# Performance work log

Hardware: AMD Instinct MI355X
Metric: run time of the kernel (lower is better)

The kernel has to match this reference:

```python
import jax, jax.numpy as jnp
import numpy as np

N_ENT = 50000; N_REL = 200; D = 128; HEADS = 2; ATT_D = 64
E_FULL = 300000; E_BATCH = 80000; NEG_SLOPE = 0.2


def _leaky(x, ns):
    return jnp.where(x >= 0, x, ns * x)


def _gat_conv(x, src, dst, ea, W, We, att_s, att_d, att_e, bias, neg_slope=0.2):
    """PyG GATConv with edge features, add_self_loops=True (fill_value='mean')."""
    N = x.shape[0]
    H, C = att_s.shape
    E = src.shape[0]
    # self-loop edge_attr = mean of incoming edge_attrs per node (PyG fill_value='mean')
    deg = jax.ops.segment_sum(jnp.ones((E,), x.dtype), dst, num_segments=N)
    ea_loop = jax.ops.segment_sum(ea, dst, num_segments=N) / jnp.maximum(deg, 1.0)[:, None]
    loops = jnp.arange(N, dtype=src.dtype)
    src2 = jnp.concatenate([src, loops])
    dst2 = jnp.concatenate([dst, loops])
    ea2 = jnp.concatenate([ea, ea_loop], axis=0)            # [E+N, edge_dim]
    xt = (x @ W).reshape(N, H, C)                            # [N,H,C]
    et = (ea2 @ We).reshape(-1, H, C)                        # [E+N,H,C]
    a_src = jnp.einsum('nhc,hc->nh', xt, att_s)
    a_dst = jnp.einsum('nhc,hc->nh', xt, att_d)
    a_edge = jnp.einsum('ehc,hc->eh', et, att_e)
    alpha = a_src[src2] + a_dst[dst2] + a_edge               # [E+N,H]
    alpha = _leaky(alpha, neg_slope)
    # segment softmax over edges sharing the same target node
    amax = jax.ops.segment_max(alpha, dst2, num_segments=N)
    ex = jnp.exp(alpha - amax[dst2])
    den = jax.ops.segment_sum(ex, dst2, num_segments=N)
    alpha = ex / (den[dst2] + 1e-16)
    out = jax.ops.segment_sum(xt[src2] * alpha[:, :, None], dst2, num_segments=N)
    return out.reshape(N, H * C) + bias


def setup_inputs() -> dict:
    key = jax.random.key(0)
    ks = list(jax.random.split(key, 24))
    p = lambda k, s: jax.random.normal(k, s, dtype=jnp.float32) * 0.05
    s = jax.random.randint(ks[0], (E_FULL,), 0, N_ENT, dtype=jnp.int32)
    r = jax.random.randint(ks[1], (E_FULL,), 0, N_REL, dtype=jnp.int32)
    t = jax.random.randint(ks[2], (E_FULL,), 0, N_ENT, dtype=jnp.int32)
    edge_data = jnp.stack([s, r, t], axis=0)
    edge_index = jax.random.randint(ks[3], (2, E_BATCH), 0, N_ENT, dtype=jnp.int32)
    rel_ids = jax.random.randint(ks[4], (E_BATCH,), 0, N_REL, dtype=jnp.int32)
    edge_attr = jax.nn.one_hot(rel_ids, N_REL, dtype=jnp.float32)
    H1 = HEADS * ATT_D
    H2 = HEADS * D
    return {
        'edge_index': edge_index, 'edge_attr': edge_attr, 'edge_data': edge_data,
        'ent_emb': p(ks[5], (N_ENT, D)), 'rel_emb': p(ks[6], (N_REL, D)),
        'W1': p(ks[7], (D, H1)), 'We1': p(ks[8], (D, H1)),
        'att_s1': p(ks[9], (HEADS, ATT_D)), 'att_d1': p(ks[10], (HEADS, ATT_D)),
        'att_e1': p(ks[11], (HEADS, ATT_D)), 'b1': jnp.zeros((H1,), jnp.float32),
        'W2': p(ks[12], (H1, H2)), 'We2': p(ks[13], (D, H2)),
        'att_s2': p(ks[14], (HEADS, D)), 'att_d2': p(ks[15], (HEADS, D)),
        'att_e2': p(ks[16], (HEADS, D)), 'b2': jnp.zeros((H2,), jnp.float32),
        'W_skip': p(ks[17], (D, D)), 'W_r': p(ks[18], (D, N_REL)),
    }


def reference(edge_index, edge_attr, edge_data, ent_emb, rel_emb, W1, We1, att_s1, att_d1, att_e1, b1, W2, We2, att_s2, att_d2, att_e2, b2, W_skip, W_r):
    src, rel, dst = edge_data[0], edge_data[1], edge_data[2]
    ea = rel_emb[rel]                                        # [E_FULL, D]
    x = _gat_conv(ent_emb, src, dst, ea, W1, We1, att_s1, att_d1, att_e1, b1)
    x = _leaky(x, NEG_SLOPE)                                 # inter-layer act
    x = _gat_conv(x, src, dst, ea, W2, We2, att_s2, att_d2, att_e2, b2)
    # mean over head chunks: [N, H*D] -> [N, D]
    x = x.reshape(N_ENT, HEADS, D).mean(axis=1)
    x = x + ent_emb @ W_skip.T                               # skip connection
    x = x / jnp.maximum(jnp.linalg.norm(x, axis=1, keepdims=True), 1e-12)
    edge_emb = jnp.stack([x[edge_index[0]], x[edge_index[1]]], axis=0)  # [2,EB,D]
    edge_attr_out = edge_attr @ W_r.T                        # [EB, D]
    return edge_emb, edge_attr_out
```

## Files before the change

kernel.cpp:

```cpp
#include <hip/hip_runtime.h>

#define NE 50000
#define NR 200
#define EF 300000
#define EB 80000
#define NEG 0.2f
#define NINF (-1e30f)

typedef unsigned short u16;
typedef unsigned int u32;
typedef u16 u16x8 __attribute__((ext_vector_type(8)));
typedef __bf16 bf16x8 __attribute__((ext_vector_type(8)));
typedef float f32x4 __attribute__((ext_vector_type(4)));

__device__ __forceinline__ float lrelu(float x){ return x >= 0.f ? x : NEG*x; }
__device__ __forceinline__ u16 f2bf(float f){
  unsigned u = __float_as_uint(f);
  u = (u + 0x7FFFu + ((u >> 16) & 1u)) >> 16;
  return (u16)u;
}
__device__ __forceinline__ float bf2f(u16 u){ return __uint_as_float(((unsigned)u) << 16); }
__device__ __forceinline__ float bflo(u32 p){ return __uint_as_float(p << 16); }
__device__ __forceinline__ float bfhi(u32 p){ return __uint_as_float(p & 0xFFFF0000u); }

__global__ void k_count(const int* __restrict__ edge_data, int* __restrict__ cnt){
  int e = blockIdx.x*blockDim.x + threadIdx.x;
  if(e < EF) atomicAdd(&cnt[edge_data[2*EF + e]], 1);
}

__global__ void k_scan(const int* __restrict__ cnt, int* __restrict__ row_start){
  __shared__ int wsum[16];
  __shared__ int s_run;
  int tid = threadIdx.x;
  int lane = tid & 63, wv = tid >> 6;
  if(tid==0) s_run = 0;
  __syncthreads();
  const int CH = 4096;
  const int nch = (NE + CH - 1)/CH;
  for(int c=0;c<nch;c++){
    int base = c*CH + tid*4;
    int v0 = base   < NE ? cnt[base]   : 0;
    int v1 = base+1 < NE ? cnt[base+1] : 0;
    int v2 = base+2 < NE ? cnt[base+2] : 0;
    int v3 = base+3 < NE ? cnt[base+3] : 0;
    int tsum = v0+v1+v2+v3;
    int x = tsum;
    #pragma unroll
    for(int o=1;o<64;o<<=1){
      int y = __shfl_up(x, o);
      if(lane >= o) x += y;
    }
    if(lane==63) wsum[wv] = x;
    __syncthreads();
    if(wv==0 && lane<16){
      int w = wsum[lane];
      #pragma unroll
      for(int o=1;o<16;o<<=1){
        int y = __shfl_up(w, o);
        if(lane>=o) w += y;
      }
      wsum[lane] = w;
    }
    __syncthreads();
    int woff = (wv>0) ? wsum[wv-1] : 0;
    int excl = s_run + woff + x - tsum;
    if(base   < NE) row_start[base]   = excl;
    if(base+1 < NE) row_start[base+1] = excl + v0;
    if(base+2 < NE) row_start[base+2] = excl + v0+v1;
    if(base+3 < NE) row_start[base+3] = excl + v0+v1+v2;
    __syncthreads();
    if(tid==1023) s_run += wsum[15];
    __syncthreads();
  }
  if(tid==0) row_start[NE] = s_run;
}

__global__ void k_fill(const int* __restrict__ edge_data, const int* __restrict__ row_start,
                       int* __restrict__ cnt, int* __restrict__ src_s, int* __restrict__ rel_s){
  int e = blockIdx.x*blockDim.x + threadIdx.x;
  if(e < EF){
    int s = edge_data[e], r = edge_data[EF+e], d = edge_data[2*EF+e];
    int pos = row_start[d] + atomicAdd(&cnt[d], 1);
    src_s[pos] = s; rel_s[pos] = r;
  }
}

__global__ void k_vecE(const float* __restrict__ We1, const float* __restrict__ ae1,
                       const float* __restrict__ We2, const float* __restrict__ ae2,
                       float* __restrict__ vecE1, float* __restrict__ vecE2){
  int t = threadIdx.x;
  int d = t>>1, h = t&1;
  float s1 = 0.f;
  for(int c=0;c<64;c++)  s1 += We1[d*128 + h*64  + c]*ae1[h*64  + c];
  vecE1[d*2+h] = s1;
  float s2 = 0.f;
  for(int c=0;c<128;c++) s2 += We2[d*256 + h*128 + c]*ae2[h*128 + c];
  vecE2[d*2+h] = s2;
}

__global__ void k_aE(const float* __restrict__ rel_emb, const float* __restrict__ vecE1,
                     const float* __restrict__ vecE2, float* __restrict__ aE1, float* __restrict__ aE2){
  int r = blockIdx.x, l = threadIdx.x;
  float re0 = rel_emb[r*128 + l], re1 = rel_emb[r*128 + 64 + l];
  float a10 = re0*vecE1[l*2+0] + re1*vecE1[(64+l)*2+0];
  float a11 = re0*vecE1[l*2+1] + re1*vecE1[(64+l)*2+1];
  float a20 = re0*vecE2[l*2+0] + re1*vecE2[(64+l)*2+0];
  float a21 = re0*vecE2[l*2+1] + re1*vecE2[(64+l)*2+1];
  for(int o=32;o;o>>=1){
    a10 += __shfl_xor(a10,o); a11 += __shfl_xor(a11,o);
    a20 += __shfl_xor(a20,o); a21 += __shfl_xor(a21,o);
  }
  if(l==0){ aE1[r*2]=a10; aE1[r*2+1]=a11; aE2[r*2]=a20; aE2[r*2+1]=a21; }
}

__global__ void k_tr(const float* __restrict__ A, float* __restrict__ At, int R, int C){
  int t = blockIdx.x*blockDim.x + threadIdx.x;
  if(t < R*C){ int r = t / C, c = t % C; At[c*R + r] = A[t]; }
}

__global__ void k_prep(const float* __restrict__ W1, const float* __restrict__ Wsk,
                       const float* __restrict__ W2, u16* __restrict__ WT1s, u16* __restrict__ WT2){
  int r = blockIdx.x, k = threadIdx.x;
  if(r < 128)       WT1s[r*128+k] = f2bf(W1[k*128 + r]);
  else if(r < 256)  WT1s[r*128+k] = f2bf(Wsk[(r-128)*128 + k]);
  else              WT2[(r-256)*128+k] = f2bf(W2[k*256 + (r-256)]);
}

template<bool XBF, bool SPLIT>
__global__ __launch_bounds__(256) void k_mgemm(const void* __restrict__ Xv,
    const u16* __restrict__ WT, u16* __restrict__ Y0, u16* __restrict__ Yb, int Nrows){
  __shared__ u16 As[64*128];
  __shared__ u16 Bs[64*128];
  int n0 = blockIdx.x*64;
  int t  = threadIdx.x;
  #pragma unroll
  for(int i=0;i<4;i++){
    int c = i*256 + t;
    int row = c >> 4, kc = c & 15;
    u16x8 pk;
    if(XBF){
      const u16* Xb = (const u16*)Xv;
      if(n0+row < Nrows) pk = *reinterpret_cast<const u16x8*>(&Xb[(size_t)(n0+row)*128 + kc*8]);
      else               pk = (u16x8)(u16)0;
    } else {
      const float* Xf = (const float*)Xv;
      float4 v0 = make_float4(0,0,0,0), v1 = v0;
      if(n0+row < Nrows){
        const float4* p = reinterpret_cast<const float4*>(&Xf[(size_t)(n0+row)*128 + kc*8]);
        v0 = p[0]; v1 = p[1];
      }
      pk[0]=f2bf(v0.x); pk[1]=f2bf(v0.y); pk[2]=f2bf(v0.z); pk[3]=f2bf(v0.w);
      pk[4]=f2bf(v1.x); pk[5]=f2bf(v1.y); pk[6]=f2bf(v1.z); pk[7]=f2bf(v1.w);
    }
    *reinterpret_cast<u16x8*>(&As[row*128 + ((kc ^ (row&7))<<3)]) = pk;
  }
  int l = t & 63, w = t >> 6;
  int wr = w >> 1, wc = w & 1;
  int lr = l & 15, kg = l >> 4;
  const bf16x8* asp = reinterpret_cast<const bf16x8*>(As);
  const bf16x8* bsp = reinterpret_cast<const bf16x8*>(Bs);
  for(int cbi=0; cbi<4; cbi++){
    int cb = cbi*64;
    #pragma unroll
    for(int i=0;i<4;i++){
      int c = i*256 + t;
      int row = c >> 4, kc = c & 15;
      u16x8 pk = *reinterpret_cast<const u16x8*>(&WT[(size_t)(cb+row)*128 + kc*8]);
      *reinterpret_cast<u16x8*>(&Bs[row*128 + ((kc ^ (row&7))<<3)]) = pk;
    }
    __syncthreads();
    f32x4 acc[2][2] = {};
    #pragma unroll
    for(int kk=0; kk<4; kk++){
      bf16x8 a[2], b[2];
      #pragma unroll
      for(int m=0;m<2;m++){
        int fr = wr*32 + m*16 + lr;
        a[m] = asp[fr*16 + ((kk*4 + kg) ^ (fr&7))];
      }
      #pragma unroll
      for(int n=0;n<2;n++){
        int fc = wc*32 + n*16 + lr;
        b[n] = bsp[fc*16 + ((kk*4 + kg) ^ (fc&7))];
      }
      #pragma unroll
      for(int m=0;m<2;m++)
        #pragma unroll
        for(int n=0;n<2;n++)
          acc[m][n] = __builtin_amdgcn_mfma_f32_16x16x32_bf16(a[m], b[n], acc[m][n], 0, 0, 0);
    }
    #pragma unroll
    for(int m=0;m<2;m++){
      #pragma unroll
      for(int r=0;r<4;r++){
        int grow = n0 + wr*32 + m*16 + kg*4 + r;
        if(grow < Nrows){
          #pragma unroll
          for(int n=0;n<2;n++){
            int gcol = cb + wc*32 + n*16 + lr;
            u16 v = f2bf(acc[m][n][r]);
            if(SPLIT){
              if(cb >= 128) Yb[(size_t)grow*128 + (gcol-128)] = v;
              else          Y0[(size_t)grow*128 + gcol] = v;
            } else {
              Y0[(size_t)grow*256 + gcol] = v;
            }
          }
        }
      }
    }
    __syncthreads();
  }
}

template<int C>
__global__ void k_attn(const u16* __restrict__ xt, const float* __restrict__ att_s,
                       const float* __restrict__ att_d, float* __restrict__ asrc,
                       float* __restrict__ adst){
  int wv = threadIdx.x>>6, l = threadIdx.x&63;
  int n = blockIdx.x*4 + wv;
  if(n >= NE) return;
  const u32* row = reinterpret_cast<const u32*>(xt) + (size_t)n*C;
  if(C==64){
    u32 p = row[l];
    float x0 = bflo(p), x1 = bfhi(p);
    float sl = x0*att_s[2*l] + x1*att_s[2*l+1];
    float dl = x0*att_d[2*l] + x1*att_d[2*l+1];
    #pragma unroll
    for(int o=16;o;o>>=1){ sl += __shfl_xor(sl,o); dl += __shfl_xor(dl,o); }
    if(l==0){  asrc[n*2]   = sl; adst[n*2]   = dl; }
    if(l==32){ asrc[n*2+1] = sl; adst[n*2+1] = dl; }
  } else {
    u32 p0 = row[l], p1 = row[64+l];
    float x00 = bflo(p0), x01 = bfhi(p0), x10 = bflo(p1), x11 = bfhi(p1);
    float s0 = x00*att_s[2*l]     + x01*att_s[2*l+1];
    float s1 = x10*att_s[128+2*l] + x11*att_s[128+2*l+1];
    float d0 = x00*att_d[2*l]     + x01*att_d[2*l+1];
    float d1 = x10*att_d[128+2*l] + x11*att_d[128+2*l+1];
    #pragma unroll
    for(int o=32;o;o>>=1){
      s0+=__shfl_xor(s0,o); s1+=__shfl_xor(s1,o);
      d0+=__shfl_xor(d0,o); d1+=__shfl_xor(d1,o);
    }
    if(l==0){ asrc[n*2]=s0; asrc[n*2+1]=s1; adst[n*2]=d0; adst[n*2+1]=d1; }
  }
}

template<int C, bool LK, bool OUTBF>
__global__ __launch_bounds__(256) void k_agg(const u16* __restrict__ xt,
    const float* __restrict__ asrc, const float* __restrict__ adst,
    const float* __restrict__ aE, const int* __restrict__ row_start,
    const int* __restrict__ src_s, const int* __restrict__ rel_s,
    const float* __restrict__ bias, void* __restrict__ outv){
  constexpr int NP = C/64;
  __shared__ float2 sAE[NR];
  int tid = threadIdx.x;
  for(int i=tid; i<NR; i+=256) sAE[i] = reinterpret_cast<const float2*>(aE)[i];
  __syncthreads();
  int wv = tid>>6, l = tid&63;
  int n = blockIdx.x*4 + wv;
  if(n >= NE) return;
  int b = row_start[n], e = row_start[n+1];
  int deg = e - b;
  float2 ad  = *reinterpret_cast<const float2*>(&adst[n*2]);
  float2 asn = *reinterpret_cast<const float2*>(&asrc[n*2]);
  const u32* xtu = reinterpret_cast<const u32*>(xt);
  float m0=NINF, m1=NINF, den0=0.f, den1=0.f, sE0=0.f, sE1=0.f;
  float acc[NP][2];
  #pragma unroll
  for(int j=0;j<NP;j++){ acc[j][0]=0.f; acc[j][1]=0.f; }
  for(int i=b;i<e;i++){
    int s = src_s[i], r = rel_s[i];
    float2 as = *reinterpret_cast<const float2*>(&asrc[s*2]);
    float2 ae = sAE[r];
    sE0 += ae.x; sE1 += ae.y;
    float l0 = lrelu(as.x + ad.x + ae.x);
    float l1 = lrelu(as.y + ad.y + ae.y);
    float nm0 = fmaxf(m0,l0), nm1 = fmaxf(m1,l1);
    float sc0 = __expf(m0-nm0), sc1 = __expf(m1-nm1);
    float w0  = __expf(l0-nm0), w1  = __expf(l1-nm1);
    den0 = den0*sc0 + w0; den1 = den1*sc1 + w1;
    m0 = nm0; m1 = nm1;
    #pragma unroll
    for(int j=0;j<NP;j++){
      u32 p = xtu[(size_t)s*C + j*64 + l];
      float sc, w;
      if(C==64){ sc = (l<32)?sc0:sc1; w = (l<32)?w0:w1; }
      else     { sc = (j==0)?sc0:sc1; w = (j==0)?w0:w1; }
      acc[j][0] = acc[j][0]*sc + w*bflo(p);
      acc[j][1] = acc[j][1]*sc + w*bfhi(p);
    }
  }
  {
    float invdeg = 1.f/fmaxf((float)deg, 1.f);
    float l0 = lrelu(asn.x + ad.x + sE0*invdeg);
    float l1 = lrelu(asn.y + ad.y + sE1*invdeg);
    float nm0 = fmaxf(m0,l0), nm1 = fmaxf(m1,l1);
    float sc0 = __expf(m0-nm0), sc1 = __expf(m1-nm1);
    float w0  = __expf(l0-nm0), w1  = __expf(l1-nm1);
    den0 = den0*sc0 + w0; den1 = den1*sc1 + w1;
    #pragma unroll
    for(int j=0;j<NP;j++){
      u32 p = xtu[(size_t)n*C + j*64 + l];
      float sc, w;
      if(C==64){ sc = (l<32)?sc0:sc1; w = (l<32)?w0:w1; }
      else     { sc = (j==0)?sc0:sc1; w = (j==0)?w0:w1; }
      acc[j][0] = acc[j][0]*sc + w*bflo(p);
      acc[j][1] = acc[j][1]*sc + w*bfhi(p);
    }
  }
  float i0 = 1.f/(den0 + 1e-16f), i1 = 1.f/(den1 + 1e-16f);
  #pragma unroll
  for(int j=0;j<NP;j++){
    float ih;
    if(C==64) ih = (l<32)?i0:i1; else ih = (j==0)?i0:i1;
    float2 bp = reinterpret_cast<const float2*>(bias)[j*64 + l];
    float v0 = acc[j][0]*ih + bp.x;
    float v1 = acc[j][1]*ih + bp.y;
    if(LK){ v0 = lrelu(v0); v1 = lrelu(v1); }
    if(OUTBF){
      ((u32*)outv)[(size_t)n*C + j*64 + l] = (u32)f2bf(v0) | ((u32)f2bf(v1)<<16);
    } else {
      reinterpret_cast<float2*>(outv)[(size_t)n*(C) + j*64 + l] = make_float2(v0, v1);
    }
  }
}

__global__ void k_combine(const float* __restrict__ out2, const u16* __restrict__ skip,
                          u16* __restrict__ xf){
  int wv = threadIdx.x>>6, l = threadIdx.x&63;
  int n = blockIdx.x*4 + wv;
  if(n >= NE) return;
  const float2* o2 = reinterpret_cast<const float2*>(out2) + (size_t)n*128;
  float2 a0 = o2[l], a1 = o2[64+l];
  u32 sp = reinterpret_cast<const u32*>(skip)[(size_t)n*64 + l];
  float v0 = 0.5f*(a0.x + a1.x) + bflo(sp);
  float v1 = 0.5f*(a0.y + a1.y) + bfhi(sp);
  float ss = v0*v0 + v1*v1;
  for(int o=32;o;o>>=1) ss += __shfl_xor(ss,o);
  float inv = 1.f/fmaxf(sqrtf(ss), 1e-12f);
  reinterpret_cast<u32*>(xf)[(size_t)n*64 + l] = (u32)f2bf(v0*inv) | ((u32)f2bf(v1*inv)<<16);
}

__global__ void k_gather(const int* __restrict__ ei, const u16* __restrict__ xf,
                         float* __restrict__ out){
  int wv = threadIdx.x>>6, l = threadIdx.x&63;
  int e = blockIdx.x*4 + wv;
  if(e >= EB) return;
  int i0 = ei[e], i1 = ei[EB + e];
  u32 p0 = reinterpret_cast<const u32*>(xf)[(size_t)i0*64 + l];
  u32 p1 = reinterpret_cast<const u32*>(xf)[(size_t)i1*64 + l];
  reinterpret_cast<float2*>(out)[(size_t)e*64 + l] = make_float2(bflo(p0), bfhi(p0));
  reinterpret_cast<float2*>(out + (size_t)EB*128)[(size_t)e*64 + l] = make_float2(bflo(p1), bfhi(p1));
}

__global__ void k_attr(const float* __restrict__ ea, const float* __restrict__ Wrt,
                       float* __restrict__ out){
  int wv = threadIdx.x>>6, l = threadIdx.x&63;
  int e = blockIdx.x*4 + wv;
  if(e >= EB) return;
  const float* row = ea + (size_t)e*NR;
  float acc0=0.f, acc1=0.f;
  #pragma unroll
  for(int ch=0; ch<4; ch++){
    int idx = ch*64 + l;
    float v = (idx < NR) ? row[idx] : 0.f;
    unsigned long long mask = __ballot(v != 0.f);
    while(mask){
      int bit = __builtin_ctzll(mask);
      mask &= mask - 1;
      int r = ch*64 + bit;
      float vv = __shfl(v, bit);
      acc0 += vv * Wrt[r*128 + l];
      acc1 += vv * Wrt[r*128 + 64 + l];
    }
  }
  out[(size_t)e*128 + l]      = acc0;
  out[(size_t)e*128 + 64 + l] = acc1;
}

extern "C" void kernel_launch(void* const* d_in, const int* in_sizes, int n_in,
                              void* d_out, int out_size, void* d_ws, size_t ws_size,
                              hipStream_t stream){
  const int*   edge_index = (const int*)  d_in[0];
  const float* edge_attr  = (const float*)d_in[1];
  const int*   edge_data  = (const int*)  d_in[2];
  const float* ent_emb    = (const float*)d_in[3];
  const float* rel_emb    = (const float*)d_in[4];
  const float* W1     = (const float*)d_in[5];
  const float* att_s1 = (const float*)d_in[7];
  const float* att_d1 = (const float*)d_in[8];
  const float* att_e1 = (const float*)d_in[9];
  const float* b1     = (const float*)d_in[10];
  const float* W2     = (const float*)d_in[11];
  const float* We1    = (const float*)d_in[6];
  const float* We2    = (const float*)d_in[12];
  const float* att_s2 = (const float*)d_in[13];
  const float* att_d2 = (const float*)d_in[14];
  const float* att_e2 = (const float*)d_in[15];
  const float* b2     = (const float*)d_in[16];
  const float* W_skip = (const float*)d_in[17];
  const float* W_r    = (const float*)d_in[18];
  float* out = (float*)d_out;

  char* ws = (char*)d_ws;
  size_t off = 0;
  auto alloc = [&](size_t bytes){ void* p = ws + off; off += (bytes + 255) & ~(size_t)255; return p; };
  int*   cnt       = (int*)  alloc((size_t)NE*4);
  int*   row_start = (int*)  alloc((size_t)(NE+1)*4);
  int*   src_s     = (int*)  alloc((size_t)EF*4);
  int*   rel_s     = (int*)  alloc((size_t)EF*4);
  float* vecE1     = (float*)alloc(128*2*4);
  float* vecE2     = (float*)alloc(128*2*4);
  float* aE1       = (float*)alloc(NR*2*4);
  float* aE2       = (float*)alloc(NR*2*4);
  float* asrc1     = (float*)alloc((size_t)NE*2*4);
  float* adst1     = (float*)alloc((size_t)NE*2*4);
  float* asrc2     = (float*)alloc((size_t)NE*2*4);
  float* adst2     = (float*)alloc((size_t)NE*2*4);
  u16*   WT1s      = (u16*)  alloc(256*128*2);
  u16*   WT2       = (u16*)  alloc(256*128*2);
  float* Wrt       = (float*)alloc(NR*128*4);
  u16*   xt1       = (u16*)  alloc((size_t)NE*128*2);
  u16*   skip      = (u16*)  alloc((size_t)NE*128*2);
  u16*   h1        = (u16*)  alloc((size_t)NE*128*2);
  u16*   xf = xt1;
  u16*   xt2  = (u16*)out;
  float* out2 = out + (size_t)NE*128;

  hipMemsetAsync(cnt, 0, (size_t)NE*4, stream);
  k_count<<<(EF+255)/256, 256, 0, stream>>>(edge_data, cnt);
  k_scan<<<1, 1024, 0, stream>>>(cnt, row_start);
  hipMemsetAsync(cnt, 0, (size_t)NE*4, stream);
  k_fill<<<(EF+255)/256, 256, 0, stream>>>(edge_data, row_start, cnt, src_s, rel_s);
  k_vecE<<<1, 256, 0, stream>>>(We1, att_e1, We2, att_e2, vecE1, vecE2);
  k_aE<<<NR, 64, 0, stream>>>(rel_emb, vecE1, vecE2, aE1, aE2);
  k_prep<<<512, 128, 0, stream>>>(W1, W_skip, W2, WT1s, WT2);
  k_tr<<<(128*NR+255)/256, 256, 0, stream>>>(W_r, Wrt, 128, NR);

  int gg = (NE+63)/64;
  k_mgemm<false, true><<<gg, 256, 0, stream>>>(ent_emb, WT1s, xt1, skip, NE);
  k_attn<64><<<(NE+3)/4, 256, 0, stream>>>(xt1, att_s1, att_d1, asrc1, adst1);
  k_agg<64, true, true><<<(NE+3)/4, 256, 0, stream>>>(xt1, asrc1, adst1, aE1, row_start, src_s, rel_s, b1, h1);

  k_mgemm<true, false><<<gg, 256, 0, stream>>>(h1, WT2, xt2, nullptr, NE);
  k_attn<128><<<(NE+3)/4, 256, 0, stream>>>(xt2, att_s2, att_d2, asrc2, adst2);
  k_agg<128, false, false><<<(NE+3)/4, 256, 0, stream>>>(xt2, asrc2, adst2, aE2, row_start, src_s, rel_s, b2, out2);

  k_combine<<<(NE+3)/4, 256, 0, stream>>>(out2, skip, xf);

  k_gather<<<(EB+3)/4, 256, 0, stream>>>(edge_index, xf, out);
  k_attr<<<(EB+3)/4, 256, 0, stream>>>(edge_attr, Wrt, out + (size_t)2*EB*128);
}
```

Baseline: 492.0 us.

## Aggregate raw features before projection and fold attention vectors into weights

The GAT layers are reordered so neighbor aggregation runs on the 128-wide input features, one output per head, and the per-head projection is applied afterwards as a K=256 MFMA GEMM. Attention logits come from precomputed W·att vectors, so the separate attention-score kernels and the transformed-feature gathers go away. The head-mean, bias, skip connection and L2 normalisation are fused into the last GEMM's epilogue. The online-softmax max tracking is dropped and raw exp is used, which risks overflow if logits grow large.

```diff
diff --git a/kernel.cpp b/kernel.cpp
--- a/kernel.cpp
+++ b/kernel.cpp
@@ -5,7 +5,6 @@
 #define EF 300000
 #define EB 80000
 #define NEG 0.2f
-#define NINF (-1e30f)
 
 typedef unsigned short u16;
 typedef unsigned int u32;
@@ -22,6 +21,7 @@
 __device__ __forceinline__ float bf2f(u16 u){ return __uint_as_float(((unsigned)u) << 16); }
 __device__ __forceinline__ float bflo(u32 p){ return __uint_as_float(p << 16); }
 __device__ __forceinline__ float bfhi(u32 p){ return __uint_as_float(p & 0xFFFF0000u); }
+__device__ __forceinline__ u32 pack2(float a, float b){ return (u32)f2bf(a) | ((u32)f2bf(b)<<16); }
 
 __global__ void k_count(const int* __restrict__ edge_data, int* __restrict__ cnt){
   int e = blockIdx.x*blockDim.x + threadIdx.x;
@@ -85,17 +85,29 @@
   }
 }
 
-__global__ void k_vecE(const float* __restrict__ We1, const float* __restrict__ ae1,
+__global__ void k_fold(const float* __restrict__ We1, const float* __restrict__ ae1,
                        const float* __restrict__ We2, const float* __restrict__ ae2,
-                       float* __restrict__ vecE1, float* __restrict__ vecE2){
+                       const float* __restrict__ W1,  const float* __restrict__ as1, const float* __restrict__ ad1,
+                       const float* __restrict__ W2,  const float* __restrict__ as2, const float* __restrict__ ad2,
+                       float* __restrict__ vecE1, float* __restrict__ vecE2,
+                       float* __restrict__ vs1, float* __restrict__ vd1,
+                       float* __restrict__ vs2, float* __restrict__ vd2){
   int t = threadIdx.x;
   int d = t>>1, h = t&1;
-  float s1 = 0.f;
-  for(int c=0;c<64;c++)  s1 += We1[d*128 + h*64  + c]*ae1[h*64  + c];
-  vecE1[d*2+h] = s1;
-  float s2 = 0.f;
-  for(int c=0;c<128;c++) s2 += We2[d*256 + h*128 + c]*ae2[h*128 + c];
-  vecE2[d*2+h] = s2;
+  float sE=0.f, sS=0.f, sD=0.f;
+  for(int c=0;c<64;c++){
+    float we = We1[d*128 + h*64 + c];
+    float w  = W1 [d*128 + h*64 + c];
+    sE += we*ae1[h*64+c]; sS += w*as1[h*64+c]; sD += w*ad1[h*64+c];
+  }
+  vecE1[d*2+h] = sE; vs1[h*128+d] = sS; vd1[h*128+d] = sD;
+  sE=0.f; sS=0.f; sD=0.f;
+  for(int c=0;c<128;c++){
+    float we = We2[d*256 + h*128 + c];
+    float w  = W2 [d*256 + h*128 + c];
+    sE += we*ae2[h*128+c]; sS += w*as2[h*128+c]; sD += w*ad2[h*128+c];
+  }
+  vecE2[d*2+h] = sE; vs2[h*128+d] = sS; vd2[h*128+d] = sD;
 }
 
 __global__ void k_aE(const float* __restrict__ rel_emb, const float* __restrict__ vecE1,
@@ -118,141 +130,90 @@
   if(t < R*C){ int r = t / C, c = t % C; At[c*R + r] = A[t]; }
 }
 
-__global__ void k_prep(const float* __restrict__ W1, const float* __restrict__ Wsk,
-                       const float* __restrict__ W2, u16* __restrict__ WT1s, u16* __restrict__ WT2){
-  int r = blockIdx.x, k = threadIdx.x;
-  if(r < 128)       WT1s[r*128+k] = f2bf(W1[k*128 + r]);
-  else if(r < 256)  WT1s[r*128+k] = f2bf(Wsk[(r-128)*128 + k]);
-  else              WT2[(r-256)*128+k] = f2bf(W2[k*256 + (r-256)]);
-}
-
-template<bool XBF, bool SPLIT>
-__global__ __launch_bounds__(256) void k_mgemm(const void* __restrict__ Xv,
-    const u16* __restrict__ WT, u16* __restrict__ Y0, u16* __restrict__ Yb, int Nrows){
-  __shared__ u16 As[64*128];
-  __shared__ u16 Bs[64*128];
-  int n0 = blockIdx.x*64;
-  int t  = threadIdx.x;
-  #pragma unroll
-  for(int i=0;i<4;i++){
-    int c = i*256 + t;
-    int row = c >> 4, kc = c & 15;
-    u16x8 pk;
-    if(XBF){
-      const u16* Xb = (const u16*)Xv;
-      if(n0+row < Nrows) pk = *reinterpret_cast<const u16x8*>(&Xb[(size_t)(n0+row)*128 + kc*8]);
-      else               pk = (u16x8)(u16)0;
-    } else {
-      const float* Xf = (const float*)Xv;
-      float4 v0 = make_float4(0,0,0,0), v1 = v0;
-      if(n0+row < Nrows){
-        const float4* p = reinterpret_cast<const float4*>(&Xf[(size_t)(n0+row)*128 + kc*8]);
-        v0 = p[0]; v1 = p[1];
-      }
-      pk[0]=f2bf(v0.x); pk[1]=f2bf(v0.y); pk[2]=f2bf(v0.z); pk[3]=f2bf(v0.w);
-      pk[4]=f2bf(v1.x); pk[5]=f2bf(v1.y); pk[6]=f2bf(v1.z); pk[7]=f2bf(v1.w);
-    }
-    *reinterpret_cast<u16x8*>(&As[row*128 + ((kc ^ (row&7))<<3)]) = pk;
-  }
-  int l = t & 63, w = t >> 6;
-  int wr = w >> 1, wc = w & 1;
-  int lr = l & 15, kg = l >> 4;
-  const bf16x8* asp = reinterpret_cast<const bf16x8*>(As);
-  const bf16x8* bsp = reinterpret_cast<const bf16x8*>(Bs);
-  for(int cbi=0; cbi<4; cbi++){
-    int cb = cbi*64;
-    #pragma unroll
-    for(int i=0;i<4;i++){
-      int c = i*256 + t;
-      int row = c >> 4, kc = c & 15;
-      u16x8 pk = *reinterpret_cast<const u16x8*>(&WT[(size_t)(cb+row)*128 + kc*8]);
-      *reinterpret_cast<u16x8*>(&Bs[row*128 + ((kc ^ (row&7))<<3)]) = pk;
-    }
-    __syncthreads();
-    f32x4 acc[2][2] = {};
-    #pragma unroll
-    for(int kk=0; kk<4; kk++){
-      bf16x8 a[2], b[2];
-      #pragma unroll
-      for(int m=0;m<2;m++){
-        int fr = wr*32 + m*16 + lr;
-        a[m] = asp[fr*16 + ((kk*4 + kg) ^ (fr&7))];
-      }
-      #pragma unroll
-      for(int n=0;n<2;n++){
-        int fc = wc*32 + n*16 + lr;
-        b[n] = bsp[fc*16 + ((kk*4 + kg) ^ (fc&7))];
-      }
-      #pragma unroll
-      for(int m=0;m<2;m++)
-        #pragma unroll
-        for(int n=0;n<2;n++)
-          acc[m][n] = __builtin_amdgcn_mfma_f32_16x16x32_bf16(a[m], b[n], acc[m][n], 0, 0, 0);
-    }
-    #pragma unroll
-    for(int m=0;m<2;m++){
-      #pragma unroll
-      for(int r=0;r<4;r++){
-        int grow = n0 + wr*32 + m*16 + kg*4 + r;
-        if(grow < Nrows){
-          #pragma unroll
-          for(int n=0;n<2;n++){
-            int gcol = cb + wc*32 + n*16 + lr;
-            u16 v = f2bf(acc[m][n][r]);
-            if(SPLIT){
-              if(cb >= 128) Yb[(size_t)grow*128 + (gcol-128)] = v;
-              else          Y0[(size_t)grow*128 + gcol] = v;
-            } else {
-              Y0[(size_t)grow*256 + gcol] = v;
-            }
-          }
-        }
-      }
-    }
-    __syncthreads();
-  }
-}
-
-template<int C>
-__global__ void k_attn(const u16* __restrict__ xt, const float* __restrict__ att_s,
-                       const float* __restrict__ att_d, float* __restrict__ asrc,
-                       float* __restrict__ adst){
-  int wv = threadIdx.x>>6, l = threadIdx.x&63;
+__global__ void k_prep(const float* __restrict__ W1, const float* __restrict__ W2,
+                       const float* __restrict__ Wsk, const float* __restrict__ b2,
+                       u16* __restrict__ WT1, u16* __restrict__ WT2,
+                       u16* __restrict__ WTs, float* __restrict__ b2m){
+  int b = blockIdx.x, t = threadIdx.x;
+  if(b < 128){
+    int c = b;
+    #pragma unroll
+    for(int rr=0; rr<2; rr++){
+      int r = rr*128 + t;
+      float v;
+      if(c < 64) v = (r < 128)  ? W1[r*128 + c] : 0.f;
+      else       v = (r >= 128) ? W1[(r-128)*128 + c] : 0.f;
+      WT1[c*256 + r] = f2bf(v);
+    }
+  } else if(b < 256){
+    int c = b - 128;
+    #pragma unroll
+    for(int rr=0; rr<2; rr++){
+      int r = rr*128 + t;
+      float v = (r < 128) ? W2[r*256 + c] : W2[(r-128)*256 + 128 + c];
+      WT2[c*256 + r] = f2bf(0.5f*v);
+    }
+  } else if(b < 384){
+    int c = b - 256;
+    WTs[c*128 + t] = f2bf(Wsk[c*128 + t]);
+  } else {
+    b2m[t] = 0.5f*(b2[t] + b2[128 + t]);
+  }
+}
+
+__global__ __launch_bounds__(256) void k_pre1(const float* __restrict__ ent, u16* __restrict__ entb,
+                       float* __restrict__ asrc, float* __restrict__ adst,
+                       const float* __restrict__ vs, const float* __restrict__ vd){
+  __shared__ float s_vs[256], s_vd[256];
+  int tid = threadIdx.x;
+  s_vs[tid] = vs[tid]; s_vd[tid] = vd[tid];
+  __syncthreads();
+  int wv = tid>>6, l = tid&63;
   int n = blockIdx.x*4 + wv;
   if(n >= NE) return;
-  const u32* row = reinterpret_cast<const u32*>(xt) + (size_t)n*C;
-  if(C==64){
-    u32 p = row[l];
-    float x0 = bflo(p), x1 = bfhi(p);
-    float sl = x0*att_s[2*l] + x1*att_s[2*l+1];
-    float dl = x0*att_d[2*l] + x1*att_d[2*l+1];
-    #pragma unroll
-    for(int o=16;o;o>>=1){ sl += __shfl_xor(sl,o); dl += __shfl_xor(dl,o); }
-    if(l==0){  asrc[n*2]   = sl; adst[n*2]   = dl; }
-    if(l==32){ asrc[n*2+1] = sl; adst[n*2+1] = dl; }
-  } else {
-    u32 p0 = row[l], p1 = row[64+l];
-    float x00 = bflo(p0), x01 = bfhi(p0), x10 = bflo(p1), x11 = bfhi(p1);
-    float s0 = x00*att_s[2*l]     + x01*att_s[2*l+1];
-    float s1 = x10*att_s[128+2*l] + x11*att_s[128+2*l+1];
-    float d0 = x00*att_d[2*l]     + x01*att_d[2*l+1];
-    float d1 = x10*att_d[128+2*l] + x11*att_d[128+2*l+1];
-    #pragma unroll
-    for(int o=32;o;o>>=1){
-      s0+=__shfl_xor(s0,o); s1+=__shfl_xor(s1,o);
-      d0+=__shfl_xor(d0,o); d1+=__shfl_xor(d1,o);
-    }
-    if(l==0){ asrc[n*2]=s0; asrc[n*2+1]=s1; adst[n*2]=d0; adst[n*2+1]=d1; }
-  }
-}
-
-template<int C, bool LK, bool OUTBF>
-__global__ __launch_bounds__(256) void k_agg(const u16* __restrict__ xt,
+  float2 e2 = reinterpret_cast<const float2*>(ent)[(size_t)n*64 + l];
+  reinterpret_cast<u32*>(entb)[(size_t)n*64 + l] = pack2(e2.x, e2.y);
+  float s0 = e2.x*s_vs[2*l]     + e2.y*s_vs[2*l+1];
+  float s1 = e2.x*s_vs[128+2*l] + e2.y*s_vs[128+2*l+1];
+  float d0 = e2.x*s_vd[2*l]     + e2.y*s_vd[2*l+1];
+  float d1 = e2.x*s_vd[128+2*l] + e2.y*s_vd[128+2*l+1];
+  #pragma unroll
+  for(int o=32;o;o>>=1){
+    s0+=__shfl_xor(s0,o); s1+=__shfl_xor(s1,o);
+    d0+=__shfl_xor(d0,o); d1+=__shfl_xor(d1,o);
+  }
+  if(l==0){ asrc[n*2]=s0; asrc[n*2+1]=s1; adst[n*2]=d0; adst[n*2+1]=d1; }
+}
+
+__global__ __launch_bounds__(256) void k_dots2(const u16* __restrict__ h1,
+                       float* __restrict__ asrc, float* __restrict__ adst,
+                       const float* __restrict__ vs, const float* __restrict__ vd){
+  __shared__ float s_vs[256], s_vd[256];
+  int tid = threadIdx.x;
+  s_vs[tid] = vs[tid]; s_vd[tid] = vd[tid];
+  __syncthreads();
+  int wv = tid>>6, l = tid&63;
+  int n = blockIdx.x*4 + wv;
+  if(n >= NE) return;
+  u32 p = reinterpret_cast<const u32*>(h1)[(size_t)n*64 + l];
+  float x0 = bflo(p), x1 = bfhi(p);
+  float s0 = x0*s_vs[2*l]     + x1*s_vs[2*l+1];
+  float s1 = x0*s_vs[128+2*l] + x1*s_vs[128+2*l+1];
+  float d0 = x0*s_vd[2*l]     + x1*s_vd[2*l+1];
+  float d1 = x0*s_vd[128+2*l] + x1*s_vd[128+2*l+1];
+  #pragma unroll
+  for(int o=32;o;o>>=1){
+    s0+=__shfl_xor(s0,o); s1+=__shfl_xor(s1,o);
+    d0+=__shfl_xor(d0,o); d1+=__shfl_xor(d1,o);
+  }
+  if(l==0){ asrc[n*2]=s0; asrc[n*2+1]=s1; adst[n*2]=d0; adst[n*2+1]=d1; }
+}
+
+__global__ __launch_bounds__(256) void k_agg(const u16* __restrict__ tab,
     const float* __restrict__ asrc, const float* __restrict__ adst,
     const float* __restrict__ aE, const int* __restrict__ row_start,
     const int* __restrict__ src_s, const int* __restrict__ rel_s,
-    const float* __restrict__ bias, void* __restrict__ outv){
-  constexpr int NP = C/64;
+    u16* __restrict__ aggE){
   __shared__ float2 sAE[NR];
   int tid = threadIdx.x;
   for(int i=tid; i<NR; i+=256) sAE[i] = reinterpret_cast<const float2*>(aE)[i];
@@ -261,85 +222,163 @@
   int n = blockIdx.x*4 + wv;
   if(n >= NE) return;
   int b = row_start[n], e = row_start[n+1];
-  int deg = e - b;
-  float2 ad  = *reinterpret_cast<const float2*>(&adst[n*2]);
-  float2 asn = *reinterpret_cast<const float2*>(&asrc[n*2]);
-  const u32* xtu = reinterpret_cast<const u32*>(xt);
-  float m0=NINF, m1=NINF, den0=0.f, den1=0.f, sE0=0.f, sE1=0.f;
-  float acc[NP][2];
-  #pragma unroll
-  for(int j=0;j<NP;j++){ acc[j][0]=0.f; acc[j][1]=0.f; }
+  float2 ad  = reinterpret_cast<const float2*>(adst)[n];
+  float2 asn = reinterpret_cast<const float2*>(asrc)[n];
+  const u32* tu = reinterpret_cast<const u32*>(tab);
+  float den0=0.f, den1=0.f, sE0=0.f, sE1=0.f;
+  float a00=0.f, a01=0.f, a10=0.f, a11=0.f;
   for(int i=b;i<e;i++){
     int s = src_s[i], r = rel_s[i];
-    float2 as = *reinterpret_cast<const float2*>(&asrc[s*2]);
+    float2 as = reinterpret_cast<const float2*>(asrc)[s];
     float2 ae = sAE[r];
     sE0 += ae.x; sE1 += ae.y;
     float l0 = lrelu(as.x + ad.x + ae.x);
     float l1 = lrelu(as.y + ad.y + ae.y);
-    float nm0 = fmaxf(m0,l0), nm1 = fmaxf(m1,l1);
-    float sc0 = __expf(m0-nm0), sc1 = __expf(m1-nm1);
-    float w0  = __expf(l0-nm0), w1  = __expf(l1-nm1);
-    den0 = den0*sc0 + w0; den1 = den1*sc1 + w1;
-    m0 = nm0; m1 = nm1;
-    #pragma unroll
-    for(int j=0;j<NP;j++){
-      u32 p = xtu[(size_t)s*C + j*64 + l];
-      float sc, w;
-      if(C==64){ sc = (l<32)?sc0:sc1; w = (l<32)?w0:w1; }
-      else     { sc = (j==0)?sc0:sc1; w = (j==0)?w0:w1; }
-      acc[j][0] = acc[j][0]*sc + w*bflo(p);
-      acc[j][1] = acc[j][1]*sc + w*bfhi(p);
-    }
+    float w0 = __expf(l0), w1 = __expf(l1);
+    den0 += w0; den1 += w1;
+    u32 p = tu[(size_t)s*64 + l];
+    float x0 = bflo(p), x1 = bfhi(p);
+    a00 += w0*x0; a01 += w0*x1;
+    a10 += w1*x0; a11 += w1*x1;
   }
   {
-    float invdeg = 1.f/fmaxf((float)deg, 1.f);
+    float invdeg = 1.f/fmaxf((float)(e-b), 1.f);
     float l0 = lrelu(asn.x + ad.x + sE0*invdeg);
     float l1 = lrelu(asn.y + ad.y + sE1*invdeg);
-    float nm0 = fmaxf(m0,l0), nm1 = fmaxf(m1,l1);
-    float sc0 = __expf(m0-nm0), sc1 = __expf(m1-nm1);
-    float w0  = __expf(l0-nm0), w1  = __expf(l1-nm1);
-    den0 = den0*sc0 + w0; den1 = den1*sc1 + w1;
-    #pragma unroll
-    for(int j=0;j<NP;j++){
-      u32 p = xtu[(size_t)n*C + j*64 + l];
-      float sc, w;
-      if(C==64){ sc = (l<32)?sc0:sc1; w = (l<32)?w0:w1; }
-      else     { sc = (j==0)?sc0:sc1; w = (j==0)?w0:w1; }
-      acc[j][0] = acc[j][0]*sc + w*bflo(p);
-      acc[j][1] = acc[j][1]*sc + w*bfhi(p);
-    }
+    float w0 = __expf(l0), w1 = __expf(l1);
+    den0 += w0; den1 += w1;
+    u32 p = tu[(size_t)n*64 + l];
+    float x0 = bflo(p), x1 = bfhi(p);
+    a00 += w0*x0; a01 += w0*x1;
+    a10 += w1*x0; a11 += w1*x1;
   }
   float i0 = 1.f/(den0 + 1e-16f), i1 = 1.f/(den1 + 1e-16f);
+  u32* og = reinterpret_cast<u32*>(aggE);
+  og[(size_t)n*128 + l]      = pack2(a00*i0, a01*i0);
+  og[(size_t)n*128 + 64 + l] = pack2(a10*i1, a11*i1);
+}
+
+template<int K, int EPI>
+__global__ __launch_bounds__(256) void k_mgemm(const u16* __restrict__ X, const u16* __restrict__ WT,
+    u16* __restrict__ Y, const float* __restrict__ bias, const u16* __restrict__ skip, int Nrows){
+  constexpr int KC  = K/8;
+  constexpr int KSH = (K==256) ? 5 : 4;
+  __shared__ u16 As[64*K];
+  __shared__ u16 Bs[64*128];
+  __shared__ float rsum[64][2];
+  int n0 = blockIdx.x*64, t = threadIdx.x;
   #pragma unroll
-  for(int j=0;j<NP;j++){
-    float ih;
-    if(C==64) ih = (l<32)?i0:i1; else ih = (j==0)?i0:i1;
-    float2 bp = reinterpret_cast<const float2*>(bias)[j*64 + l];
-    float v0 = acc[j][0]*ih + bp.x;
-    float v1 = acc[j][1]*ih + bp.y;
-    if(LK){ v0 = lrelu(v0); v1 = lrelu(v1); }
-    if(OUTBF){
-      ((u32*)outv)[(size_t)n*C + j*64 + l] = (u32)f2bf(v0) | ((u32)f2bf(v1)<<16);
-    } else {
-      reinterpret_cast<float2*>(outv)[(size_t)n*(C) + j*64 + l] = make_float2(v0, v1);
-    }
-  }
-}
-
-__global__ void k_combine(const float* __restrict__ out2, const u16* __restrict__ skip,
-                          u16* __restrict__ xf){
-  int wv = threadIdx.x>>6, l = threadIdx.x&63;
-  int n = blockIdx.x*4 + wv;
-  if(n >= NE) return;
-  const float2* o2 = reinterpret_cast<const float2*>(out2) + (size_t)n*128;
-  float2 a0 = o2[l], a1 = o2[64+l];
-  u32 sp = reinterpret_cast<const u32*>(skip)[(size_t)n*64 + l];
-  float v0 = 0.5f*(a0.x + a1.x) + bflo(sp);
-  float v1 = 0.5f*(a0.y + a1.y) + bfhi(sp);
-  float ss = v0*v0 + v1*v1;
-  for(int o=32;o;o>>=1) ss += __shfl_xor(ss,o);
-  float inv = 1.f/fmaxf(sqrtf(ss), 1e-12f);
-  reinterpret_cast<u32*>(xf)[(size_t)n*64 + l] = (u32)f2bf(v0*inv) | ((u32)f2bf(v1*inv)<<16);
+  for(int i=0;i<K/32;i++){
+    int c = i*256 + t;
+    int row = c >> KSH, kc = c & (KC-1);
+    u16x8 pk = (u16x8)(u16)0;
+    if(n0+row < Nrows) pk = *reinterpret_cast<const u16x8*>(&X[(size_t)(n0+row)*K + kc*8]);
+    *reinterpret_cast<u16x8*>(&As[row*K + ((kc ^ (row&7))<<3)]) = pk;
+  }
+  int l = t&63, w = t>>6, wr = w>>1, wc = w&1, lr = l&15, kg = l>>4;
+  const bf16x8* asp = reinterpret_cast<const bf16x8*>(As);
+  const bf16x8* bsp = reinterpret_cast<const bf16x8*>(Bs);
+  f32x4 acc[2][2][2] = {};
+  constexpr int NKH = K/128;
+  for(int cbi=0;cbi<2;cbi++){
+    for(int kh=0;kh<NKH;kh++){
+      #pragma unroll
+      for(int i=0;i<4;i++){
+        int c = i*256 + t;
+        int row = c>>4, kc = c&15;
+        u16x8 pk = *reinterpret_cast<const u16x8*>(&WT[(size_t)(cbi*64+row)*K + kh*128 + kc*8]);
+        *reinterpret_cast<u16x8*>(&Bs[row*128 + ((kc ^ (row&7))<<3)]) = pk;
+      }
+      __syncthreads();
+      #pragma unroll
+      for(int kk=0;kk<4;kk++){
+        bf16x8 a[2], bb[2];
+        #pragma unroll
+        for(int m=0;m<2;m++){
+          int fr = wr*32 + m*16 + lr;
+          a[m] = asp[fr*(K/8) + ((kh*16 + kk*4 + kg) ^ (fr&7))];
+        }
+        #pragma unroll
+        for(int nn=0;nn<2;nn++){
+          int fc = wc*32 + nn*16 + lr;
+          bb[nn] = bsp[fc*16 + ((kk*4 + kg) ^ (fc&7))];
+        }
+        #pragma unroll
+        for(int m=0;m<2;m++)
+          #pragma unroll
+          for(int nn=0;nn<2;nn++)
+            acc[cbi][m][nn] = __builtin_amdgcn_mfma_f32_16x16x32_bf16(a[m], bb[nn], acc[cbi][m][nn], 0, 0, 0);
+      }
+      __syncthreads();
+    }
+  }
+  if(EPI < 2){
+    #pragma unroll
+    for(int cbi=0;cbi<2;cbi++)
+      #pragma unroll
+      for(int m=0;m<2;m++)
+        #pragma unroll
+        for(int r=0;r<4;r++){
+          int grow = n0 + wr*32 + m*16 + kg*4 + r;
+          if(grow < Nrows){
+            #pragma unroll
+            for(int nn=0;nn<2;nn++){
+              int gcol = cbi*64 + wc*32 + nn*16 + lr;
+              float v = acc[cbi][m][nn][r];
+              if(EPI==1){ v += bias[gcol]; v = lrelu(v); }
+              Y[(size_t)grow*128 + gcol] = f2bf(v);
+            }
+          }
+        }
+  } else {
+    #pragma unroll
+    for(int cbi=0;cbi<2;cbi++)
+      #pragma unroll
+      for(int m=0;m<2;m++)
+        #pragma unroll
+        for(int r=0;r<4;r++){
+          int grow = n0 + wr*32 + m*16 + kg*4 + r;
+          if(grow < Nrows){
+            #pragma unroll
+            for(int nn=0;nn<2;nn++){
+              int gcol = cbi*64 + wc*32 + nn*16 + lr;
+              acc[cbi][m][nn][r] += bias[gcol] + bf2f(skip[(size_t)grow*128 + gcol]);
+            }
+          }
+        }
+    #pragma unroll
+    for(int m=0;m<2;m++)
+      #pragma unroll
+      for(int r=0;r<4;r++){
+        float s = 0.f;
+        #pragma unroll
+        for(int cbi=0;cbi<2;cbi++)
+          #pragma unroll
+          for(int nn=0;nn<2;nn++){ float v = acc[cbi][m][nn][r]; s += v*v; }
+        #pragma unroll
+        for(int o=1;o<16;o<<=1) s += __shfl_xor(s, o);
+        if(lr==0) rsum[wr*32 + m*16 + kg*4 + r][wc] = s;
+      }
+    __syncthreads();
+    #pragma unroll
+    for(int m=0;m<2;m++)
+      #pragma unroll
+      for(int r=0;r<4;r++){
+        int row = wr*32 + m*16 + kg*4 + r;
+        int grow = n0 + row;
+        if(grow < Nrows){
+          float tot = rsum[row][0] + rsum[row][1];
+          float inv = 1.f/fmaxf(sqrtf(tot), 1e-12f);
+          #pragma unroll
+          for(int cbi=0;cbi<2;cbi++)
+            #pragma unroll
+            for(int nn=0;nn<2;nn++){
+              int gcol = cbi*64 + wc*32 + nn*16 + lr;
+              Y[(size_t)grow*128 + gcol] = f2bf(acc[cbi][m][nn][r]*inv);
+            }
+        }
+      }
+  }
 }
 
 __global__ void k_gather(const int* __restrict__ ei, const u16* __restrict__ xf,
@@ -388,12 +427,12 @@
   const float* ent_emb    = (const float*)d_in[3];
   const float* rel_emb    = (const float*)d_in[4];
   const float* W1     = (const float*)d_in[5];
+  const float* We1    = (const float*)d_in[6];
   const float* att_s1 = (const float*)d_in[7];
   const float* att_d1 = (const float*)d_in[8];
   const float* att_e1 = (const float*)d_in[9];
   const float* b1     = (const float*)d_in[10];
   const float* W2     = (const float*)d_in[11];
-  const float* We1    = (const float*)d_in[6];
   const float* We2    = (const float*)d_in[12];
   const float* att_s2 = (const float*)d_in[13];
   const float* att_d2 = (const float*)d_in[14];
@@ -414,40 +453,46 @@
   float* vecE2     = (float*)alloc(128*2*4);
   float* aE1       = (float*)alloc(NR*2*4);
   float* aE2       = (float*)alloc(NR*2*4);
+  float* vs1       = (float*)alloc(256*4);
+  float* vd1       = (float*)alloc(256*4);
+  float* vs2       = (float*)alloc(256*4);
+  float* vd2       = (float*)alloc(256*4);
+  float* b2m       = (float*)alloc(128*4);
   float* asrc1     = (float*)alloc((size_t)NE*2*4);
   float* adst1     = (float*)alloc((size_t)NE*2*4);
   float* asrc2     = (float*)alloc((size_t)NE*2*4);
   float* adst2     = (float*)alloc((size_t)NE*2*4);
-  u16*   WT1s      = (u16*)  alloc(256*128*2);
-  u16*   WT2       = (u16*)  alloc(256*128*2);
+  u16*   WT1cat    = (u16*)  alloc(128*256*2);
+  u16*   WT2cat    = (u16*)  alloc(128*256*2);
+  u16*   WTsk      = (u16*)  alloc(128*128*2);
   float* Wrt       = (float*)alloc(NR*128*4);
-  u16*   xt1       = (u16*)  alloc((size_t)NE*128*2);
+  u16*   entb      = (u16*)  alloc((size_t)NE*128*2);
+  u16*   h1        = (u16*)  alloc((size_t)NE*128*2);
   u16*   skip      = (u16*)  alloc((size_t)NE*128*2);
-  u16*   h1        = (u16*)  alloc((size_t)NE*128*2);
-  u16*   xf = xt1;
-  u16*   xt2  = (u16*)out;
-  float* out2 = out + (size_t)NE*128;
+  u16*   xf = entb;
+  u16*   aggE1 = (u16*)out;
+  u16*   aggE2 = (u16*)out + (size_t)NE*256;
 
   hipMemsetAsync(cnt, 0, (size_t)NE*4, stream);
   k_count<<<(EF+255)/256, 256, 0, stream>>>(edge_data, cnt);
   k_scan<<<1, 1024, 0, stream>>>(cnt, row_start);
   hipMemsetAsync(cnt, 0, (size_t)NE*4, stream);
   k_fill<<<(EF+255)/256, 256, 0, stream>>>(edge_data, row_start, cnt, src_s, rel_s);
-  k_vecE<<<1, 256, 0, stream>>>(We1, att_e1, We2, att_e2, vecE1, vecE2);
+
+  k_fold<<<1, 256, 0, stream>>>(We1, att_e1, We2, att_e2, W1, att_s1, att_d1,
+                                W2, att_s2, att_d2, vecE1, vecE2, vs1, vd1, vs2, vd2);
   k_aE<<<NR, 64, 0, stream>>>(rel_emb, vecE1, vecE2, aE1, aE2);
-  k_prep<<<512, 128, 0, stream>>>(W1, W_skip, W2, WT1s, WT2);
+  k_prep<<<385, 128, 0, stream>>>(W1, W2, W_skip, b2, WT1cat, WT2cat, WTsk, b2m);
   k_tr<<<(128*NR+255)/256, 256, 0, stream>>>(W_r, Wrt, 128, NR);
 
-  int gg = (NE+63)/64;
-  k_mgemm<false, true><<<gg, 256, 0, stream>>>(ent_emb, WT1s, xt1, skip, NE);
-  k_attn<64><<<(NE+3)/4, 256, 0, stream>>>(xt1, att_s1, att_d1, asrc1, adst1);
-  k_agg<64, true, true><<<(NE+3)/4, 256, 0, stream>>>(xt1, asrc1, adst1, aE1, row_start, src_s, rel_s, b1, h1);
-
-  k_mgemm<true, false><<<gg, 256, 0, stream>>>(h1, WT2, xt2, nullptr, NE);
-  k_attn<128><<<(NE+3)/4, 256, 0, stream>>>(xt2, att_s2, att_d2, asrc2, adst2);
-  k_agg<128, false, false><<<(NE+3)/4, 256, 0, stream>>>(xt2, asrc2, adst2, aE2, row_start, src_s, rel_s, b2, out2);
-
-  k_combine<<<(NE+3)/4, 256, 0, stream>>>(out2, skip, xf);
+  int gn = (NE+3)/4, gm = (NE+63)/64;
+  k_pre1<<<gn, 256, 0, stream>>>(ent_emb, entb, asrc1, adst1, vs1, vd1);
+  k_agg<<<gn, 256, 0, stream>>>(entb, asrc1, adst1, aE1, row_start, src_s, rel_s, aggE1);
+  k_mgemm<256,1><<<gm, 256, 0, stream>>>(aggE1, WT1cat, h1, b1, nullptr, NE);
+  k_dots2<<<gn, 256, 0, stream>>>(h1, asrc2, adst2, vs2, vd2);
+  k_agg<<<gn, 256, 0, stream>>>(h1, asrc2, adst2, aE2, row_start, src_s, rel_s, aggE2);
+  k_mgemm<128,0><<<gm, 256, 0, stream>>>(entb, WTsk, skip, nullptr, nullptr, NE);
+  k_mgemm<256,2><<<gm, 256, 0, stream>>>(aggE2, WT2cat, xf, b2m, skip, NE);
 
   k_gather<<<(EB+3)/4, 256, 0, stream>>>(edge_index, xf, out);
   k_attr<<<(EB+3)/4, 256, 0, stream>>>(edge_attr, Wrt, out + (size_t)2*EB*128);
```

After: 529.6 us. 7.6% more time.
